# Performance work log

Hardware: AMD Instinct MI355X
Metric: run time of the kernel (lower is better)

The kernel has to match this reference:

```python
import jax, jax.numpy as jnp
import numpy as np

N_VOX = 500_000
C = 128
HID = 4 * C
RES = 128  # voxel grid resolution
K_OFFS = 27


def _build_sparse_coords_and_neighbors(seed=0):
    rng = np.random.default_rng(seed)
    lin = rng.choice(RES ** 3, size=N_VOX, replace=False)
    z = lin // (RES * RES)
    y = (lin // RES) % RES
    x = lin % RES
    # padded grid (RES+2)^3 so boundary lookups are in-bounds
    P = RES + 2
    grid = -np.ones(P * P * P, dtype=np.int64)
    z1, y1, x1 = z + 1, y + 1, x + 1
    grid[z1 * P * P + y1 * P + x1] = np.arange(N_VOX)
    offs = np.array([[dz, dy, dx] for dz in (-1, 0, 1) for dy in (-1, 0, 1) for dx in (-1, 0, 1)], dtype=np.int64)  # [27,3]
    nz = z1[:, None] + offs[None, :, 0]
    ny = y1[:, None] + offs[None, :, 1]
    nx = x1[:, None] + offs[None, :, 2]
    nbr = grid[nz * P * P + ny * P + nx]  # [N,27], -1 if neighbor voxel inactive
    return nbr.astype(np.int32)


def setup_inputs() -> dict:
    key = jax.random.key(0)
    ks = jax.random.split(key, 8)
    nbr = _build_sparse_coords_and_neighbors()
    scale = 0.02
    return {
        "feats": jax.random.normal(ks[0], (N_VOX, C), jnp.float32),
        "neighbor_idx": jnp.asarray(nbr),
        "conv_w": jax.random.normal(ks[1], (K_OFFS, C, C), jnp.float32) * scale,
        "conv_b": jax.random.normal(ks[2], (C,), jnp.float32) * scale,
        "ln_g": jnp.ones((C,), jnp.float32),
        "ln_b": jnp.zeros((C,), jnp.float32),
        "w1": jax.random.normal(ks[3], (C, HID), jnp.float32) * scale,
        "b1": jax.random.normal(ks[4], (HID,), jnp.float32) * scale,
        "w2": jax.random.normal(ks[5], (HID, C), jnp.float32) * scale,
        "b2": jax.random.normal(ks[6], (C,), jnp.float32) * scale,
    }


def _forward(feats, neighbor_idx, conv_w, conv_b, ln_g, ln_b, w1, b1, w2, b2):
    n, c = feats.shape
    # submanifold sparse conv3d: pad a zero row for missing (-1) neighbors
    f_pad = jnp.concatenate([feats, jnp.zeros((1, c), feats.dtype)], axis=0)
    idx = jnp.where(neighbor_idx < 0, n, neighbor_idx)  # [N,27]
    h = jnp.broadcast_to(conv_b, (n, c))
    for k in range(K_OFFS):  # fixed small kernel-offset loop; per-offset gather + GEMM
        h = h + f_pad[idx[:, k]] @ conv_w[k]
    # LayerNorm32 (fp32 math), eps=1e-6, affine
    h32 = h.astype(jnp.float32)
    mu = h32.mean(-1, keepdims=True)
    var = h32.var(-1, keepdims=True)
    hn = ((h32 - mu) * jax.lax.rsqrt(var + 1e-6) * ln_g + ln_b).astype(feats.dtype)
    # MLP: Linear -> SiLU -> Linear
    m = jax.nn.silu(hn @ w1 + b1) @ w2 + b2
    # residual h + x on sparse feats
    return m + feats


def reference(feats, neighbor_idx, conv_w, conv_b, ln_g, ln_b, w1, b1, w2, b2):
    return _forward(feats, neighbor_idx, conv_w, conv_b, ln_g, ln_b, w1, b1, w2, b2)
```

## Files before the change

kernel.cpp:

```cpp
#include <hip/hip_runtime.h>
#include <stdint.h>

#define NVOX 500000

typedef float  f32x4  __attribute__((ext_vector_type(4)));
typedef short  short8 __attribute__((ext_vector_type(8)));

__device__ __forceinline__ short f2bf(float x){
  unsigned u = __float_as_uint(x);
  unsigned r = (u + 0x7fffu + ((u >> 16) & 1u)) >> 16;
  return (short)r;
}

__device__ __forceinline__ void gload_lds16(const void* g, void* l){
  __builtin_amdgcn_global_load_lds(
      (const __attribute__((address_space(1))) unsigned int*)(uintptr_t)g,
      (__attribute__((address_space(3))) unsigned int*)(unsigned int)(uintptr_t)l,
      16, 0, 0);
}

__global__ void cast_feats_kernel(const float* __restrict__ f, short* __restrict__ t){
  long i = ((long)blockIdx.x * 256 + threadIdx.x) * 8;
  float4 a = *(const float4*)(f + i);
  float4 b = *(const float4*)(f + i + 4);
  short8 o = { f2bf(a.x), f2bf(a.y), f2bf(a.z), f2bf(a.w),
               f2bf(b.x), f2bf(b.y), f2bf(b.z), f2bf(b.w) };
  *(short8*)(t + i) = o;
}

__global__ void prep_weights_kernel(const float* __restrict__ cw, const float* __restrict__ w1,
                                    const float* __restrict__ w2,
                                    short* __restrict__ cw_sw, short* __restrict__ w1_sw,
                                    short* __restrict__ w2_sw){
  int t = blockIdx.x * 256 + threadIdx.x;
  if (t < 55296){
    int k = t >> 11, rem = t & 2047;
    int nf = rem >> 8, ks = (rem >> 6) & 3, l = rem & 63;
    int g = l >> 4, c = l & 15;
    short8 o;
    #pragma unroll
    for (int j = 0; j < 8; j++){
      int kk = ks*32 + g*8 + j;
      o[j] = f2bf(cw[(k*128 + kk)*128 + nf*16 + c]);
    }
    *(short8*)(cw_sw + (size_t)t*8) = o;
  } else if (t < 63488){
    int u = t - 55296;
    int nf = u >> 8, ks = (u >> 6) & 3, l = u & 63;
    int g = l >> 4, c = l & 15;
    short8 o;
    #pragma unroll
    for (int j = 0; j < 8; j++){
      int kk = ks*32 + g*8 + j;
      o[j] = f2bf(w1[kk*512 + nf*16 + c]);
    }
    *(short8*)(w1_sw + (size_t)u*8) = o;
  } else {
    int u = t - 63488;
    int ch = u >> 10, rem = u & 1023;
    int nf = rem >> 7, ks2 = (rem >> 6) & 1, l = u & 63;
    int g = l >> 4, c = l & 15;
    short8 o;
    #pragma unroll
    for (int j = 0; j < 8; j++){
      int k = ch*64 + ks2*32 + g*8 + j;
      o[j] = f2bf(w2[k*128 + nf*16 + c]);
    }
    *(short8*)(w2_sw + (size_t)u*8) = o;
  }
}

template<bool TBL>
__global__ __launch_bounds__(256, 2)
void conv_ln_kernel(const short* __restrict__ table, const float* __restrict__ feats,
                    const int* __restrict__ nbr, const short* __restrict__ cw_sw,
                    const float* __restrict__ conv_b, const float* __restrict__ ln_g,
                    const float* __restrict__ ln_b, short* __restrict__ hn16){
  __shared__ __align__(16) short lds_b[2][16384];
  const int tid = threadIdx.x;
  const int lane = tid & 63, wv = tid >> 6;
  const int l15 = lane & 15, lg = lane >> 4;
  const int rowbase = blockIdx.x * 256 + wv * 64;

  f32x4 acc[4][8];
  #pragma unroll
  for (int m = 0; m < 4; m++)
    #pragma unroll
    for (int n = 0; n < 8; n++)
      acc[m][n] = f32x4{0.f, 0.f, 0.f, 0.f};

  {
    const char* src = (const char*)cw_sw;
    char* dst = (char*)&lds_b[0][0];
    #pragma unroll
    for (int i = 0; i < 8; i++){ int off = i*4096 + tid*16; gload_lds16(src+off, dst+off); }
  }

  for (int k = 0; k < 27; k++){
    const int buf = k & 1;
    __syncthreads();
    if (k + 1 < 27){
      const char* src = (const char*)cw_sw + (size_t)(k+1)*32768;
      char* dst = (char*)&lds_b[buf ^ 1][0];
      #pragma unroll
      for (int i = 0; i < 8; i++){ int off = i*4096 + tid*16; gload_lds16(src+off, dst+off); }
    }
    int idxr[4];
    #pragma unroll
    for (int m = 0; m < 4; m++){
      int row = rowbase + m*16 + l15;
      row = row < NVOX ? row : NVOX - 1;
      int id = nbr[row*27 + k];
      idxr[m] = TBL ? (id < 0 ? NVOX : id) : id;
    }
    const short* bbase = &lds_b[buf][0];
    #pragma unroll
    for (int ks = 0; ks < 4; ks++){
      short8 af[4];
      #pragma unroll
      for (int m = 0; m < 4; m++){
        if constexpr (TBL){
          af[m] = *(const short8*)(table + (size_t)idxr[m]*128 + ks*32 + lg*8);
        } else {
          if (idxr[m] < 0){
            af[m] = short8{0,0,0,0,0,0,0,0};
          } else {
            const float* p = feats + (size_t)idxr[m]*128 + ks*32 + lg*8;
            float4 x = *(const float4*)p;
            float4 y = *(const float4*)(p + 4);
            af[m] = short8{ f2bf(x.x), f2bf(x.y), f2bf(x.z), f2bf(x.w),
                            f2bf(y.x), f2bf(y.y), f2bf(y.z), f2bf(y.w) };
          }
        }
      }
      #pragma unroll
      for (int n = 0; n < 8; n++){
        short8 b = *(const short8*)(bbase + ((n*4 + ks)*64 + lane)*8);
        #pragma unroll
        for (int m = 0; m < 4; m++)
          acc[m][n] = __builtin_amdgcn_mfma_f32_16x16x32_bf16(af[m], b, acc[m][n], 0, 0, 0);
      }
    }
  }

  float cb[8], g8[8], be[8];
  #pragma unroll
  for (int n = 0; n < 8; n++){
    cb[n] = conv_b[n*16 + l15];
    g8[n] = ln_g[n*16 + l15];
    be[n] = ln_b[n*16 + l15];
  }
  #pragma unroll
  for (int m = 0; m < 4; m++){
    #pragma unroll
    for (int r = 0; r < 4; r++){
      float s = 0.f, s2 = 0.f;
      #pragma unroll
      for (int n = 0; n < 8; n++){
        float h = acc[m][n][r] + cb[n];
        acc[m][n][r] = h;
        s += h; s2 += h*h;
      }
      #pragma unroll
      for (int msk = 1; msk < 16; msk <<= 1){
        s  += __shfl_xor(s,  msk);
        s2 += __shfl_xor(s2, msk);
      }
      float mu  = s  * 0.0078125f;
      float var = s2 * 0.0078125f - mu*mu;
      float rs  = rsqrtf(var + 1e-6f);
      int row = rowbase + m*16 + lg*4 + r;
      if (row < NVOX){
        #pragma unroll
        for (int n = 0; n < 8; n++){
          float hv = (acc[m][n][r] - mu) * rs * g8[n] + be[n];
          hn16[(size_t)row*128 + n*16 + l15] = f2bf(hv);
        }
      }
    }
  }
}

__global__ __launch_bounds__(256, 2)
void mlp_kernel(const short* __restrict__ hn16, const float* __restrict__ feats,
                const short* __restrict__ w1_sw, const short* __restrict__ w2_sw,
                const float* __restrict__ b1, const float* __restrict__ b2,
                float* __restrict__ out){
  __shared__ __align__(16) short lds_w[2][16384];
  __shared__ __align__(16) short lds_act[4*2048];
  const int tid = threadIdx.x;
  const int lane = tid & 63, wv = tid >> 6;
  const int l15 = lane & 15, lg = lane >> 4;
  const int rowbase = blockIdx.x * 128 + wv * 32;
  short* actw = &lds_act[wv * 2048];

  f32x4 acc2[2][8];
  #pragma unroll
  for (int m = 0; m < 2; m++)
    #pragma unroll
    for (int n = 0; n < 8; n++)
      acc2[m][n] = f32x4{0.f, 0.f, 0.f, 0.f};

  int rowg[2];
  #pragma unroll
  for (int m = 0; m < 2; m++){
    int row = rowbase + m*16 + l15;
    rowg[m] = row < NVOX ? row : NVOX - 1;
  }

  short8 a1[4][2];
  #pragma unroll
  for (int ks = 0; ks < 4; ks++)
    #pragma unroll
    for (int m = 0; m < 2; m++)
      a1[ks][m] = *(const short8*)(hn16 + (size_t)rowg[m]*128 + ks*32 + lg*8);

  {
    const char* s1 = (const char*)w1_sw;
    const char* s2 = (const char*)w2_sw;
    char* dst = (char*)&lds_w[0][0];
    #pragma unroll
    for (int i = 0; i < 4; i++){ int off = i*4096 + tid*16; gload_lds16(s1+off, dst+off); }
    #pragma unroll
    for (int i = 0; i < 4; i++){ int off = i*4096 + tid*16; gload_lds16(s2+off, dst+16384+off); }
  }

  for (int ch = 0; ch < 8; ch++){
    const int buf = ch & 1;
    __syncthreads();
    if (ch + 1 < 8){
      const char* s1 = (const char*)w1_sw + (size_t)(ch+1)*16384;
      const char* s2 = (const char*)w2_sw + (size_t)(ch+1)*16384;
      char* dst = (char*)&lds_w[buf ^ 1][0];
      #pragma unroll
      for (int i = 0; i < 4; i++){ int off = i*4096 + tid*16; gload_lds16(s1+off, dst+off); }
      #pragma unroll
      for (int i = 0; i < 4; i++){ int off = i*4096 + tid*16; gload_lds16(s2+off, dst+16384+off); }
    }
    const short* w1c = &lds_w[buf][0];
    const short* w2c = &lds_w[buf][8192];

    #pragma unroll
    for (int n = 0; n < 4; n++){
      f32x4 p0 = f32x4{0.f,0.f,0.f,0.f};
      f32x4 p1 = f32x4{0.f,0.f,0.f,0.f};
      #pragma unroll
      for (int ks = 0; ks < 4; ks++){
        short8 b = *(const short8*)(w1c + ((n*4 + ks)*64 + lane)*8);
        p0 = __builtin_amdgcn_mfma_f32_16x16x32_bf16(a1[ks][0], b, p0, 0, 0, 0);
        p1 = __builtin_amdgcn_mfma_f32_16x16x32_bf16(a1[ks][1], b, p1, 0, 0, 0);
      }
      float bb1 = b1[ch*64 + n*16 + l15];
      #pragma unroll
      for (int r = 0; r < 4; r++){
        float x0 = p0[r] + bb1;
        float x1 = p1[r] + bb1;
        float s0 = x0 / (1.f + __expf(-x0));
        float s1 = x1 / (1.f + __expf(-x1));
        int r0 = lg*4 + r;
        int r1 = 16 + lg*4 + r;
        actw[(r0*64 + n*16 + l15) ^ ((r0 & 7) << 3)] = f2bf(s0);
        actw[(r1*64 + n*16 + l15) ^ ((r1 & 7) << 3)] = f2bf(s1);
      }
    }

    #pragma unroll
    for (int ks2 = 0; ks2 < 2; ks2++){
      short8 a2[2];
      #pragma unroll
      for (int m = 0; m < 2; m++){
        int rowloc = m*16 + l15;
        a2[m] = *(const short8*)(actw + ((rowloc*64 + ks2*32 + lg*8) ^ ((rowloc & 7) << 3)));
      }
      #pragma unroll
      for (int n = 0; n < 8; n++){
        short8 b = *(const short8*)(w2c + ((n*2 + ks2)*64 + lane)*8);
        #pragma unroll
        for (int m = 0; m < 2; m++)
          acc2[m][n] = __builtin_amdgcn_mfma_f32_16x16x32_bf16(a2[m], b, acc2[m][n], 0, 0, 0);
      }
    }
  }

  float bb2[8];
  #pragma unroll
  for (int n = 0; n < 8; n++) bb2[n] = b2[n*16 + l15];
  #pragma unroll
  for (int m = 0; m < 2; m++)
    #pragma unroll
    for (int n = 0; n < 8; n++)
      #pragma unroll
      for (int r = 0; r < 4; r++){
        int row = rowbase + m*16 + lg*4 + r;
        if (row < NVOX){
          size_t ci = (size_t)row*128 + n*16 + l15;
          out[ci] = acc2[m][n][r] + bb2[n] + feats[ci];
        }
      }
}

extern "C" void kernel_launch(void* const* d_in, const int* in_sizes, int n_in,
                              void* d_out, int out_size, void* d_ws, size_t ws_size,
                              hipStream_t stream){
  const float* feats = (const float*)d_in[0];
  const int*   nbr   = (const int*)  d_in[1];
  const float* cw    = (const float*)d_in[2];
  const float* cb    = (const float*)d_in[3];
  const float* lng   = (const float*)d_in[4];
  const float* lnb   = (const float*)d_in[5];
  const float* w1    = (const float*)d_in[6];
  const float* b1    = (const float*)d_in[7];
  const float* w2    = (const float*)d_in[8];
  const float* b2    = (const float*)d_in[9];
  float* out = (float*)d_out;

  char* ws = (char*)d_ws;
  const size_t TABLE_B = (size_t)(NVOX + 1) * 256;
  const size_t HN_B    = (size_t)NVOX * 256;
  const size_t CW_B    = 55296u * 16u;
  const size_t W1_B    = 8192u * 16u;
  const size_t W2_B    = 8192u * 16u;
  const size_t need_full = TABLE_B + HN_B + CW_B + W1_B + W2_B;

  if (ws_size >= need_full){
    short* table = (short*)ws;
    short* hn16  = (short*)(ws + TABLE_B);
    short* cw_sw = (short*)(ws + TABLE_B + HN_B);
    short* w1_sw = (short*)(ws + TABLE_B + HN_B + CW_B);
    short* w2_sw = (short*)(ws + TABLE_B + HN_B + CW_B + W1_B);

    cast_feats_kernel<<<31250, 256, 0, stream>>>(feats, table);
    hipMemsetAsync((void*)(table + (size_t)NVOX * 128), 0, 256, stream);
    prep_weights_kernel<<<280, 256, 0, stream>>>(cw, w1, w2, cw_sw, w1_sw, w2_sw);
    conv_ln_kernel<true><<<1954, 256, 0, stream>>>(table, feats, nbr, cw_sw, cb, lng, lnb, hn16);
    mlp_kernel<<<3907, 256, 0, stream>>>(hn16, feats, w1_sw, w2_sw, b1, b2, out);
  } else {
    short* hn16  = (short*)ws;
    short* cw_sw = (short*)(ws + HN_B);
    short* w1_sw = (short*)(ws + HN_B + CW_B);
    short* w2_sw = (short*)(ws + HN_B + CW_B + W1_B);

    prep_weights_kernel<<<280, 256, 0, stream>>>(cw, w1, w2, cw_sw, w1_sw, w2_sw);
    conv_ln_kernel<false><<<1954, 256, 0, stream>>>(nullptr, feats, nbr, cw_sw, cb, lng, lnb, hn16);
    mlp_kernel<<<3907, 256, 0, stream>>>(hn16, feats, w1_sw, w2_sw, b1, b2, out);
  }
}
```

Before: 959.8 us.

## Transpose neighbor indices and software-pipeline gathers in sparse conv kernel

Adds a prep kernel that transposes the neighbor index table to offset-major layout, pre-multiplied by the row stride with missing neighbors mapped to the zero row. A new conv+LayerNorm kernel reads these coalesced indices and prefetches the next offset's indices and first feature slice one iteration ahead, overlapping gather latency with MFMA work. This costs an extra kernel launch, about 54 MB of extra workspace traffic for the transposed indices, and more registers, which could lower occupancy.

Result: faster. 926.2 us (-3.5%).

```diff
diff --git a/kernel.cpp b/kernel.cpp
--- a/kernel.cpp
+++ b/kernel.cpp
@@ -2,6 +2,8 @@
 #include <stdint.h>
 
 #define NVOX 500000
+#define NPAD 500224
+#define ZERO_OFF (NVOX * 128)
 
 typedef float  f32x4  __attribute__((ext_vector_type(4)));
 typedef short  short8 __attribute__((ext_vector_type(8)));
@@ -26,6 +28,24 @@
   short8 o = { f2bf(a.x), f2bf(a.y), f2bf(a.z), f2bf(a.w),
                f2bf(b.x), f2bf(b.y), f2bf(b.z), f2bf(b.w) };
   *(short8*)(t + i) = o;
+}
+
+__global__ void prep_nbr_kernel(const int* __restrict__ nbr, int* __restrict__ nbrT){
+  __shared__ int lds_n[6912];
+  const int tid = threadIdx.x;
+  const long base = (long)blockIdx.x * 6912;
+  #pragma unroll
+  for (int i = 0; i < 27; i++){
+    long g = base + i*256 + tid;
+    lds_n[i*256 + tid] = (g < (long)NVOX*27) ? nbr[g] : -1;
+  }
+  __syncthreads();
+  const int row = blockIdx.x * 256 + tid;
+  #pragma unroll
+  for (int k = 0; k < 27; k++){
+    int id = lds_n[tid*27 + k];
+    nbrT[(size_t)k*NPAD + row] = (id < 0 ? NVOX : id) * 128;
+  }
 }
 
 __global__ void prep_weights_kernel(const float* __restrict__ cw, const float* __restrict__ w1,
@@ -67,6 +87,128 @@
       o[j] = f2bf(w2[k*128 + nf*16 + c]);
     }
     *(short8*)(w2_sw + (size_t)u*8) = o;
+  }
+}
+
+__global__ __launch_bounds__(256, 2)
+void conv_ln_pf_kernel(const short* __restrict__ table, const int* __restrict__ nbrT,
+                       const short* __restrict__ cw_sw,
+                       const float* __restrict__ conv_b, const float* __restrict__ ln_g,
+                       const float* __restrict__ ln_b, short* __restrict__ hn16){
+  __shared__ __align__(16) short lds_b[2][16384];
+  const int tid = threadIdx.x;
+  const int lane = tid & 63, wv = tid >> 6;
+  const int l15 = lane & 15, lg = lane >> 4;
+  const int rowbase = blockIdx.x * 256 + wv * 64;
+  const int rowi = rowbase + l15;
+
+  f32x4 acc[4][8];
+  #pragma unroll
+  for (int m = 0; m < 4; m++)
+    #pragma unroll
+    for (int n = 0; n < 8; n++)
+      acc[m][n] = f32x4{0.f, 0.f, 0.f, 0.f};
+
+  int idx_c[4], idx_n[4];
+  #pragma unroll
+  for (int m = 0; m < 4; m++) idx_c[m] = nbrT[rowi + m*16];
+  #pragma unroll
+  for (int m = 0; m < 4; m++) idx_n[m] = nbrT[NPAD + rowi + m*16];
+  short8 afp[4];
+  #pragma unroll
+  for (int m = 0; m < 4; m++)
+    afp[m] = *(const short8*)(table + (size_t)(unsigned)idx_c[m] + lg*8);
+  {
+    const char* src = (const char*)cw_sw;
+    char* dst = (char*)&lds_b[0][0];
+    #pragma unroll
+    for (int i = 0; i < 8; i++){ int off = i*4096 + tid*16; gload_lds16(src+off, dst+off); }
+  }
+
+  for (int k = 0; k < 27; k++){
+    const int buf = k & 1;
+    __syncthreads();
+    if (k + 1 < 27){
+      const char* src = (const char*)cw_sw + (size_t)(k+1)*32768;
+      char* dst = (char*)&lds_b[buf ^ 1][0];
+      #pragma unroll
+      for (int i = 0; i < 8; i++){ int off = i*4096 + tid*16; gload_lds16(src+off, dst+off); }
+    }
+    int idx_n2[4];
+    #pragma unroll
+    for (int m = 0; m < 4; m++)
+      idx_n2[m] = (k + 2 < 27) ? nbrT[(size_t)(k+2)*NPAD + rowi + m*16] : ZERO_OFF;
+    short8 af1[4], af2[4], af3[4];
+    #pragma unroll
+    for (int m = 0; m < 4; m++)
+      af1[m] = *(const short8*)(table + (size_t)(unsigned)idx_c[m] + 32 + lg*8);
+    #pragma unroll
+    for (int m = 0; m < 4; m++)
+      af2[m] = *(const short8*)(table + (size_t)(unsigned)idx_c[m] + 64 + lg*8);
+    #pragma unroll
+    for (int m = 0; m < 4; m++)
+      af3[m] = *(const short8*)(table + (size_t)(unsigned)idx_c[m] + 96 + lg*8);
+    short8 afp_n[4];
+    #pragma unroll
+    for (int m = 0; m < 4; m++)
+      afp_n[m] = *(const short8*)(table + (size_t)(unsigned)idx_n[m] + lg*8);
+
+    const short* bbase = &lds_b[buf][0];
+    #pragma unroll
+    for (int ks = 0; ks < 4; ks++){
+      #pragma unroll
+      for (int n = 0; n < 8; n++){
+        short8 b = *(const short8*)(bbase + ((n*4 + ks)*64 + lane)*8);
+        #pragma unroll
+        for (int m = 0; m < 4; m++){
+          short8 a = (ks == 0) ? afp[m] : (ks == 1) ? af1[m] : (ks == 2) ? af2[m] : af3[m];
+          acc[m][n] = __builtin_amdgcn_mfma_f32_16x16x32_bf16(a, b, acc[m][n], 0, 0, 0);
+        }
+      }
+    }
+    #pragma unroll
+    for (int m = 0; m < 4; m++){
+      afp[m] = afp_n[m];
+      idx_c[m] = idx_n[m];
+      idx_n[m] = idx_n2[m];
+    }
+  }
+
+  float cb[8], g8[8], be[8];
+  #pragma unroll
+  for (int n = 0; n < 8; n++){
+    cb[n] = conv_b[n*16 + l15];
+    g8[n] = ln_g[n*16 + l15];
+    be[n] = ln_b[n*16 + l15];
+  }
+  #pragma unroll
+  for (int m = 0; m < 4; m++){
+    #pragma unroll
+    for (int r = 0; r < 4; r++){
+      float s = 0.f, s2 = 0.f;
+      #pragma unroll
+      for (int n = 0; n < 8; n++){
+        float h = acc[m][n][r] + cb[n];
+        acc[m][n][r] = h;
+        s += h; s2 += h*h;
+      }
+      #pragma unroll
+      for (int msk = 1; msk < 16; msk <<= 1){
+        s  += __shfl_xor(s,  msk);
+        s2 += __shfl_xor(s2, msk);
+      }
+      float mu  = s  * 0.0078125f;
+      float var = s2 * 0.0078125f - mu*mu;
+      float rs  = rsqrtf(var + 1e-6f);
+      int row = rowbase + m*16 + lg*4 + r;
+      if (row < NVOX){
+        #pragma unroll
+        for (int n = 0; n < 8; n++){
+          float hv = (acc[m][n][r] - mu) * rs * g8[n] + be[n];
+          hn16[(size_t)row*128 + n*16 + l15] = f2bf(hv);
+        }
+      }
+    }
   }
 }
 
@@ -320,9 +462,25 @@
   const size_t CW_B    = 55296u * 16u;
   const size_t W1_B    = 8192u * 16u;
   const size_t W2_B    = 8192u * 16u;
+  const size_t NBRT_B  = (size_t)27 * NPAD * 4;
   const size_t need_full = TABLE_B + HN_B + CW_B + W1_B + W2_B;
-
-  if (ws_size >= need_full){
+  const size_t need_pf   = need_full + NBRT_B;
+
+  if (ws_size >= need_pf){
+    short* table = (short*)ws;
+    short* hn16  = (short*)(ws + TABLE_B);
+    short* cw_sw = (short*)(ws + TABLE_B + HN_B);
+    short* w1_sw = (short*)(ws + TABLE_B + HN_B + CW_B);
+    short* w2_sw = (short*)(ws + TABLE_B + HN_B + CW_B + W1_B);
+    int*   nbrT  = (int*)  (ws + need_full);
+
+    cast_feats_kernel<<<31250, 256, 0, stream>>>(feats, table);
+    hipMemsetAsync((void*)(table + (size_t)NVOX * 128), 0, 256, stream);
+    prep_nbr_kernel<<<1954, 256, 0, stream>>>(nbr, nbrT);
+    prep_weights_kernel<<<280, 256, 0, stream>>>(cw, w1, w2, cw_sw, w1_sw, w2_sw);
+    conv_ln_pf_kernel<<<1954, 256, 0, stream>>>(table, nbrT, cw_sw, cb, lng, lnb, hn16);
+    mlp_kernel<<<3907, 256, 0, stream>>>(hn16, feats, w1_sw, w2_sw, b1, b2, out);
+  } else if (ws_size >= need_full){
     short* table = (short*)ws;
     short* hn16  = (short*)(ws + TABLE_B);
     short* cw_sw = (short*)(ws + TABLE_B + HN_B);
```
